# Kernel optimization log

Hardware: AMD Instinct MI355X
Metric: run time of the kernel (lower is better)

Reference implementation:

```python
import jax, jax.numpy as jnp
import numpy as np

NF = 64        # num_feat
B = 4
H = 128
W = 128
KH = KW = 3
K = KH * KW    # 9 kernel taps
DG = 1         # deformable_groups


def conv3x3(x, w, b):
    y = jax.lax.conv_general_dilated(
        x, w, window_strides=(1, 1), padding=((1, 1), (1, 1)),
        dimension_numbers=('NCHW', 'OIHW', 'NCHW'))
    return y + b[None, :, None, None]


def lrelu(x):
    return jnp.where(x >= 0, x, 0.1 * x)


def modulated_deform_conv(x, offset, mask, w, b):
    """DCNv2: bilinear gather at learned offsets, modulated by sigmoid mask.
    x: [B,C,H,W], offset: [B,2K,H,W] (y,x interleaved per tap), mask: [B,K,H,W].
    stride=1, padding=1, dilation=1, zero outside boundaries (mmcv semantics).
    """
    Bb, C, Hh, Ww = x.shape
    off = offset.reshape(Bb, K, 2, Hh, Ww)
    oy, ox = off[:, :, 0], off[:, :, 1]
    ki = (jnp.arange(K) // KW - 1).astype(x.dtype)  # dilation*i - pad
    kj = (jnp.arange(K) % KW - 1).astype(x.dtype)
    py = jnp.arange(Hh, dtype=x.dtype)[None, None, :, None] + ki[None, :, None, None] + oy  # [B,K,H,W]
    px = jnp.arange(Ww, dtype=x.dtype)[None, None, None, :] + kj[None, :, None, None] + ox
    y0 = jnp.floor(py)
    x0 = jnp.floor(px)
    wy1 = py - y0
    wx1 = px - x0
    x_flat = x.reshape(Bb, C, Hh * Ww)

    def gather(yi, xi):
        valid = (yi >= 0) & (yi < Hh) & (xi >= 0) & (xi < Ww)
        yc = jnp.clip(yi, 0, Hh - 1).astype(jnp.int32)
        xc = jnp.clip(xi, 0, Ww - 1).astype(jnp.int32)
        idx = (yc * Ww + xc).reshape(Bb, -1)                      # [B, K*H*W]
        g = jax.vmap(lambda xf, i: jnp.take(xf, i, axis=1))(x_flat, idx)  # [B,C,K*H*W]
        g = g.reshape(Bb, C, K, Hh, Ww)
        return g * valid[:, None].astype(x.dtype)

    v00 = gather(y0, x0)
    v01 = gather(y0, x0 + 1)
    v10 = gather(y0 + 1, x0)
    v11 = gather(y0 + 1, x0 + 1)
    wy = wy1[:, None]
    wx = wx1[:, None]
    samp = (v00 * (1 - wy) * (1 - wx) + v01 * (1 - wy) * wx
            + v10 * wy * (1 - wx) + v11 * wy * wx)                # [B,C,K,H,W]
    samp = samp * mask[:, None]
    out = jnp.einsum('bckhw,ock->bohw', samp, w.reshape(w.shape[0], C, K))
    return out + b[None, :, None, None]


def setup_inputs() -> dict:
    key = jax.random.key(0)
    ks = jax.random.split(key, 12)
    s = 0.05
    return {
        'nbr_feat_l': jax.random.normal(ks[0], (B, NF, H, W), jnp.float32),
        'ref_feat_l': jax.random.normal(ks[1], (B, NF, H, W), jnp.float32),
        'w1': jax.random.normal(ks[2], (NF, 2 * NF, 3, 3), jnp.float32) * s,
        'b1': jnp.zeros((NF,), jnp.float32),
        'w2': jax.random.normal(ks[3], (NF, NF, 3, 3), jnp.float32) * s,
        'b2': jnp.zeros((NF,), jnp.float32),
        'w3': jax.random.normal(ks[4], (NF, NF, 3, 3), jnp.float32) * s,
        'b3': jnp.zeros((NF,), jnp.float32),
        'w_off': jax.random.normal(ks[5], (DG * 3 * K, NF, 3, 3), jnp.float32) * s,
        'b_off': jnp.zeros((DG * 3 * K,), jnp.float32),
        'w_dcn': jax.random.normal(ks[6], (NF, NF, 3, 3), jnp.float32) * s,
        'b_dcn': jnp.zeros((NF,), jnp.float32),
    }


def reference(nbr_feat_l, ref_feat_l, w1, b1, w2, b2, w3, b3, w_off, b_off, w_dcn, b_dcn):
    o = jnp.concatenate([nbr_feat_l, ref_feat_l], axis=1)
    o = lrelu(conv3x3(o, w1, b1))
    o = lrelu(conv3x3(o, w2, b2))
    o = lrelu(conv3x3(o, w3, b3))
    out = conv3x3(o, w_off, b_off)                      # [B, 27, H, W]
    o1, o2, m = jnp.split(out, 3, axis=1)
    offset = 15 * jnp.tanh(jnp.concatenate([o1, o2], axis=1))  # [B, 18, H, W]
    mask = jax.nn.sigmoid(m)                                   # [B, 9, H, W]
    feat = lrelu(modulated_deform_conv(nbr_feat_l, offset, mask, w_dcn, b_dcn))
    return feat, offset, mask
```

## Files before the change

kernel.cpp:

```cpp
#include <hip/hip_runtime.h>
#include <math.h>


typedef _Float16 h8 __attribute__((ext_vector_type(8)));
typedef _Float16 h4 __attribute__((ext_vector_type(4)));
typedef _Float16 h2 __attribute__((ext_vector_type(2)));
typedef float f4 __attribute__((ext_vector_type(4)));

__global__ __launch_bounds__(256) void setup_kernel(
    const float* __restrict__ nbr, const float* __restrict__ refp,
    const float* __restrict__ w1, const float* __restrict__ w2,
    const float* __restrict__ w3, const float* __restrict__ w_off,
    const float* __restrict__ w_dcn,
    _Float16* __restrict__ X1, _Float16* __restrict__ X2,
    _Float16* __restrict__ B64, _Float16* __restrict__ C64,
    _Float16* __restrict__ wF1, _Float16* __restrict__ wF2,
    _Float16* __restrict__ wF3, _Float16* __restrict__ wFo,
    _Float16* __restrict__ wFd) {
  __shared__ float t[64 * 65];
  int bid = blockIdx.x;
  int tid = threadIdx.x;
  if (bid < 792) {
    int i = bid * 256 + tid;
    if (i < 73728) {
      int j = i;
      int icw = j & 31; int t1 = j >> 5; int oc = t1 & 63; int t2 = t1 >> 6;
      int ch = t2 & 3; int tap = t2 >> 2; int ic = ch * 32 + icw;
      wF1[j] = (_Float16)w1[(oc * 128 + ic) * 9 + tap];
    } else if (i < 110592) {
      int j = i - 73728;
      int icw = j & 31; int t1 = j >> 5; int oc = t1 & 63; int t2 = t1 >> 6;
      int ch = t2 & 1; int tap = t2 >> 1; int ic = ch * 32 + icw;
      wF2[j] = (_Float16)w2[(oc * 64 + ic) * 9 + tap];
    } else if (i < 147456) {
      int j = i - 110592;
      int icw = j & 31; int t1 = j >> 5; int oc = t1 & 63; int t2 = t1 >> 6;
      int ch = t2 & 1; int tap = t2 >> 1; int ic = ch * 32 + icw;
      wF3[j] = (_Float16)w3[(oc * 64 + ic) * 9 + tap];
    } else if (i < 165888) {
      int jj = i - 147456;
      int pc = jj >> 10;
      int mt = (jj >> 9) & 1;
      int Lx = (jj >> 3) & 63;
      int e  = jj & 7;
      int tap = pc >> 1, c = pc & 1;
      int oc = mt * 16 + (Lx & 15);
      int ic = c * 32 + (Lx >> 4) * 8 + e;
      float v = (oc < 27) ? w_off[(oc * 64 + ic) * 9 + tap] : 0.f;
      wFo[jj] = (_Float16)v;
    } else if (i < 202752) {
      int jj = i - 165888;
      int ks = jj >> 11;
      int mt = (jj >> 9) & 3;
      int Lx = (jj >> 3) & 63;
      int e  = jj & 7;
      int k = ks >> 1, s = ks & 1;
      int oc = mt * 16 + (Lx & 15);
      int ch = s * 32 + (Lx >> 4) * 8 + e;
      wFd[jj] = (_Float16)w_dcn[(oc * 64 + ch) * 9 + k];
    }
    return;
  }
  if (bid < 1050) {
    int i = (bid - 792) * 256 + tid;
    int bufi = i / 16512;
    int j = i - bufi * 16512;
    int b = j / 4128;
    int r = j - b * 4128;
    int p = r >> 3; int cg = r & 7;
    int row, col;
    if (p < 130)      { row = 0;   col = p; }
    else if (p < 260) { row = 129; col = p - 130; }
    else if (p < 388) { row = 1 + (p - 260); col = 0; }
    else              { row = 1 + (p - 388); col = 129; }
    _Float16* dst = (bufi == 0) ? X1 : (bufi == 1) ? X2 : (bufi == 2) ? B64 : C64;
    uint4 z; z.x = z.y = z.z = z.w = 0u;
    *(uint4*)(dst + ((size_t)(b * 130 + row) * 130 + col) * 64 + cg * 8) = z;
    return;
  }
  int j = bid - 1050;
  int half = j & 1;
  int y = (j >> 1) & 127;
  int b = (j >> 8) & 3;
  int src = j >> 10;
  const float* sp = src ? refp : nbr;
  _Float16* dst = src ? X2 : X1;
  for (int l = tid; l < 64 * 64; l += 256) {
    int c = l >> 6, gx = l & 63;
    t[c * 65 + gx] = sp[(((size_t)b * 64 + c) << 14) + (y << 7) + half * 64 + gx];
  }
  __syncthreads();
  unsigned* dstU = (unsigned*)dst;
  for (int l = tid; l < 64 * 32; l += 256) {
    int pxl = l >> 5, c2 = l & 31;
    union { _Float16 h[2]; unsigned u; } pk;
    pk.h[0] = (_Float16)t[(2 * c2) * 65 + pxl];
    pk.h[1] = (_Float16)t[(2 * c2 + 1) * 65 + pxl];
    dstU[((size_t)(b * 130 + y + 1) * 130 + 1 + half * 64 + pxl) * 32 + c2] = pk.u;
  }
}

template <int NCH, bool SPLIT>
__global__ __launch_bounds__(128, 4) void conv3x3_lds_kernel(
    const _Float16* __restrict__ X1, const _Float16* __restrict__ X2,
    const _Float16* __restrict__ W, const float* __restrict__ bias,
    _Float16* __restrict__ outP) {
  __shared__ _Float16 Lb[3 * 72 * 64];
  int tid = threadIdx.x;
  int wv = tid >> 6, L = tid & 63;
  int lm = L & 15, lq = L >> 4;
  int bid = blockIdx.x;
  int xcd = bid & 7, j = bid >> 3;
  int half = j & 1;
  int y = (xcd << 4) | ((j >> 1) & 15);
  int b = j >> 5;
  int px0 = half * 64;

  auto stage = [&](const _Float16* Xsrc) {
    const char* Xb = (const char*)Xsrc;
    size_t rb0 = ((size_t)(b * 130 + y) * 130 + px0) * 128;
    for (int i = wv; i < 27; i += 2) {
      int o = i * 1024 + L * 16;
      int row = o / 9216;
      int orow = o - row * 9216;
      int px = orow >> 7;
      int c2 = (orow >> 4) & 7;
      size_t src = rb0 + (size_t)row * 16640 + (size_t)(px << 7) + (((c2 ^ (px & 7))) << 4);
      __builtin_amdgcn_global_load_lds(
          (const __attribute__((address_space(1))) void*)(Xb + src),
          (__attribute__((address_space(3))) void*)((char*)Lb + i * 1024), 16, 0, 0);
    }
  };

  f4 acc[2][4];
#pragma unroll
  for (int m = 0; m < 2; ++m)
#pragma unroll
    for (int n = 0; n < 4; ++n) acc[m][n] = (f4)0.f;

  auto compute = [&](int cbase) {
#pragma unroll
    for (int ci = 0; ci < 2; ++ci) {
      int c = cbase + ci;
#pragma unroll
      for (int tg = 0; tg < 3; ++tg) {
        h8 a[6];
#pragma unroll
        for (int t = 0; t < 3; ++t) {
          int tap = tg * 3 + t;
          const _Float16* wp = W + (size_t)((tap * NCH + c) * 64 + wv * 32 + lm) * 32 + lq * 8;
          a[2 * t]     = *(const h8*)(wp);
          a[2 * t + 1] = *(const h8*)(wp + 512);
        }
#pragma unroll
        for (int t = 0; t < 3; ++t) {
          int tap = tg * 3 + t;
          const int dy = tap / 3, dx = tap % 3;
          h8 bf[4];
#pragma unroll
          for (int g = 0; g < 4; ++g) {
            int pxcol = g * 16 + lm + dx;
            int chunk = (ci * 4 + lq) ^ (pxcol & 7);
            int off = dy * 9216 + (pxcol << 7) + (chunk << 4);
            bf[g] = *(const h8*)((const char*)Lb + off);
          }
#pragma unroll
          for (int g = 0; g < 4; ++g) {
            acc[0][g] = __builtin_amdgcn_mfma_f32_16x16x32_f16(a[2 * t], bf[g], acc[0][g], 0, 0, 0);
            acc[1][g] = __builtin_amdgcn_mfma_f32_16x16x32_f16(a[2 * t + 1], bf[g], acc[1][g], 0, 0, 0);
          }
        }
      }
    }
  };

  stage(X1);
  asm volatile("s_waitcnt vmcnt(0)" ::: "memory");
  __syncthreads();
  compute(0);
  if (SPLIT) {
    __syncthreads();
    stage(X2);
    asm volatile("s_waitcnt vmcnt(0)" ::: "memory");
    __syncthreads();
    compute(2);
  }

  const size_t obase = ((size_t)(b * 130 + (y + 1)) * 130 + 1 + px0) * 64;
#pragma unroll
  for (int mt = 0; mt < 2; ++mt)
#pragma unroll
    for (int nt = 0; nt < 4; ++nt) {
      int px = nt * 16 + lm;
      h4 pk;
#pragma unroll
      for (int r = 0; r < 4; ++r) {
        int oc = wv * 32 + mt * 16 + lq * 4 + r;
        float v = acc[mt][nt][r] + bias[oc];
        v = (v >= 0.f) ? v : 0.1f * v;
        pk[r] = (_Float16)v;
      }
      *(h4*)(outP + obase + (size_t)px * 64 + wv * 32 + mt * 16 + lq * 4) = pk;
    }
}

__global__ __launch_bounds__(256, 4) void off_dcn_kernel(
    const _Float16* __restrict__ Xc, const _Float16* __restrict__ Xs,
    const _Float16* __restrict__ Wo, const float* __restrict__ bo,
    const _Float16* __restrict__ wD, const float* __restrict__ bd,
    float* __restrict__ off_out, float* __restrict__ mask_out,
    float* __restrict__ out) {
  __shared__ float Soff[4][16][28];
  int tid = threadIdx.x;
  int wv = tid >> 6, L = tid & 63;
  int lm = L & 15, lq = L >> 4;
  int lq8 = lq * 8;
  int g = blockIdx.x;
  int xcd = g & 7;
  int r0 = g >> 3;
  int half = r0 & 1;
  int y = (xcd << 4) | ((r0 >> 1) & 15);
  int b = r0 >> 5;
  int px0 = half * 64 + wv * 16;
  int gpx = px0 + lm;
  int hw = (y << 7) + gpx;
  int rb = b * 130;

  {
    f4 oa[2];
    oa[0] = (f4)0.f; oa[1] = (f4)0.f;
#pragma unroll
    for (int c = 0; c < 2; ++c) {
      const void* pB[9];
#pragma unroll
      for (int tap = 0; tap < 9; ++tap) {
        const int dy = tap / 3 - 1, dx = tap % 3 - 1;
        pB[tap] = (const void*)(Xc + ((size_t)((rb + (y + 1 + dy)) * 130) + (1 + dx) + px0 + lm) * 64
                                   + c * 32 + lq8);
      }
      h8 bq[9];
      asm volatile(
          "global_load_dwordx4 %0, %9, off\n\t"
          "global_load_dwordx4 %1, %10, off\n\t"
          "global_load_dwordx4 %2, %11, off\n\t"
          "global_load_dwordx4 %3, %12, off\n\t"
          "global_load_dwordx4 %4, %13, off\n\t"
          "global_load_dwordx4 %5, %14, off\n\t"
          "global_load_dwordx4 %6, %15, off\n\t"
          "global_load_dwordx4 %7, %16, off\n\t"
          "global_load_dwordx4 %8, %17, off\n\t"
          "s_waitcnt vmcnt(0)"
          : "=&v"(bq[0]), "=&v"(bq[1]), "=&v"(bq[2]), "=&v"(bq[3]), "=&v"(bq[4]),
            "=&v"(bq[5]), "=&v"(bq[6]), "=&v"(bq[7]), "=&v"(bq[8])
          : "v"(pB[0]), "v"(pB[1]), "v"(pB[2]), "v"(pB[3]), "v"(pB[4]),
            "v"(pB[5]), "v"(pB[6]), "v"(pB[7]), "v"(pB[8])
          : "memory");
#pragma unroll
      for (int tap = 0; tap < 9; ++tap) {
        const _Float16* wp = Wo + (size_t)(tap * 2 + c) * 1024 + L * 8;
        h8 a0 = *(const h8*)(wp);
        h8 a1 = *(const h8*)(wp + 512);
        oa[0] = __builtin_amdgcn_mfma_f32_16x16x32_f16(a0, bq[tap], oa[0], 0, 0, 0);
        oa[1] = __builtin_amdgcn_mfma_f32_16x16x32_f16(a1, bq[tap], oa[1], 0, 0, 0);
      }
    }
#pragma unroll
    for (int mt = 0; mt < 2; ++mt)
#pragma unroll
      for (int r = 0; r < 4; ++r) {
        int oc = mt * 16 + lq * 4 + r;
        if (oc < 18) {
          float v = 15.f * tanhf(oa[mt][r] + bo[oc]);
          off_out[((b * 18 + oc) << 14) + hw] = v;
          Soff[wv][lm][oc] = v;
        } else if (oc < 27) {
          float v = 1.f / (1.f + expf(-(oa[mt][r] + bo[oc])));
          mask_out[((b * 9 + (oc - 18)) << 14) + hw] = v;
          Soff[wv][lm][oc] = v;
        }
      }
  }

  f4 acc[4];
#pragma unroll
  for (int mm = 0; mm < 4; ++mm) acc[mm] = (f4)0.f;

  const char* Xb = (const char*)Xs;
  const int cbL = lq8 * 2;

#pragma unroll
  for (int gp = 0; gp < 3; ++gp) {
    float soy[3], sox[3], som[3];
#pragma unroll
    for (int t = 0; t < 3; ++t) {
      const int k = gp * 3 + t;
      soy[t] = Soff[wv][lm][2 * k];
      sox[t] = Soff[wv][lm][2 * k + 1];
      som[t] = Soff[wv][lm][18 + k];
    }
    int ro0[3], ro1[3], co0[3], co1[3];
    h2 Wc00[3], Wc01[3], Wc10[3], Wc11[3];
#pragma unroll
    for (int t = 0; t < 3; ++t) {
      const int k = gp * 3 + t;
      const int kr = k / 3, kc = k - kr * 3;
      float py = (float)(y + kr - 1) + soy[t];
      float pxf = (float)(gpx + kc - 1) + sox[t];
      float fy = floorf(py), fx = floorf(pxf);
      float wy = py - fy, wx = pxf - fx;
      int y0 = (int)fy, x0 = (int)fx;
      int y1 = y0 + 1, x1 = x0 + 1;
      float vy0 = ((unsigned)y0 < 128u) ? 1.f : 0.f;
      float vy1 = ((unsigned)y1 < 128u) ? 1.f : 0.f;
      float vx0 = ((unsigned)x0 < 128u) ? 1.f : 0.f;
      float vx1 = ((unsigned)x1 < 128u) ? 1.f : 0.f;
      float ey = 1.f - wy, ex = 1.f - wx;
      float mk = som[t];
      _Float16 w00 = (_Float16)(ey * ex * mk * vy0 * vx0);
      _Float16 w01 = (_Float16)(ey * wx * mk * vy0 * vx1);
      _Float16 w10 = (_Float16)(wy * ex * mk * vy1 * vx0);
      _Float16 w11 = (_Float16)(wy * wx * mk * vy1 * vx1);
      Wc00[t] = (h2){w00, w00}; Wc01[t] = (h2){w01, w01};
      Wc10[t] = (h2){w10, w10}; Wc11[t] = (h2){w11, w11};
      int y0c = min(max(y0, 0), 127) + 1, y1c = min(max(y1, 0), 127) + 1;
      int x0c = min(max(x0, 0), 127) + 1, x1c = min(max(x1, 0), 127) + 1;
      ro0[t] = (rb + y0c) * 16640;
      ro1[t] = (rb + y1c) * 16640;
      co0[t] = x0c * 128;
      co1[t] = x1c * 128;
    }
#pragma unroll
    for (int s = 0; s < 2; ++s) {
      const int cb2 = cbL + s * 64;
      const void* A[12];
#pragma unroll
      for (int t = 0; t < 3; ++t) {
        A[t * 4 + 0] = (const void*)(Xb + (ro0[t] + co0[t] + cb2));
        A[t * 4 + 1] = (const void*)(Xb + (ro0[t] + co1[t] + cb2));
        A[t * 4 + 2] = (const void*)(Xb + (ro1[t] + co0[t] + cb2));
        A[t * 4 + 3] = (const void*)(Xb + (ro1[t] + co1[t] + cb2));
      }
      h8 gv[12];
      asm volatile(
          "global_load_dwordx4 %0, %12, off\n\t"
          "global_load_dwordx4 %1, %13, off\n\t"
          "global_load_dwordx4 %2, %14, off\n\t"
          "global_load_dwordx4 %3, %15, off\n\t"
          "global_load_dwordx4 %4, %16, off\n\t"
          "global_load_dwordx4 %5, %17, off\n\t"
          "global_load_dwordx4 %6, %18, off\n\t"
          "global_load_dwordx4 %7, %19, off\n\t"
          "global_load_dwordx4 %8, %20, off\n\t"
          "global_load_dwordx4 %9, %21, off\n\t"
          "global_load_dwordx4 %10, %22, off\n\t"
          "global_load_dwordx4 %11, %23, off\n\t"
          "s_waitcnt vmcnt(0)"
          : "=&v"(gv[0]), "=&v"(gv[1]), "=&v"(gv[2]), "=&v"(gv[3]),
            "=&v"(gv[4]), "=&v"(gv[5]), "=&v"(gv[6]), "=&v"(gv[7]),
            "=&v"(gv[8]), "=&v"(gv[9]), "=&v"(gv[10]), "=&v"(gv[11])
          : "v"(A[0]), "v"(A[1]), "v"(A[2]), "v"(A[3]),
            "v"(A[4]), "v"(A[5]), "v"(A[6]), "v"(A[7]),
            "v"(A[8]), "v"(A[9]), "v"(A[10]), "v"(A[11])
          : "memory");
#pragma unroll
      for (int t = 0; t < 3; ++t) {
        const int k = gp * 3 + t;
        h8 bv;
#pragma unroll
        for (int j2 = 0; j2 < 4; ++j2) {
          h2 a  = {gv[t * 4 + 0][2 * j2], gv[t * 4 + 0][2 * j2 + 1]};
          h2 bb = {gv[t * 4 + 1][2 * j2], gv[t * 4 + 1][2 * j2 + 1]};
          h2 cc = {gv[t * 4 + 2][2 * j2], gv[t * 4 + 2][2 * j2 + 1]};
          h2 dd = {gv[t * 4 + 3][2 * j2], gv[t * 4 + 3][2 * j2 + 1]};
          h2 r = a * Wc00[t];
          r += bb * Wc01[t];
          r += cc * Wc10[t];
          r += dd * Wc11[t];
          bv[2 * j2] = r[0];
          bv[2 * j2 + 1] = r[1];
        }
        const _Float16* wp = wD + (size_t)(k * 2 + s) * 2048 + L * 8;
        acc[0] = __builtin_amdgcn_mfma_f32_16x16x32_f16(*(const h8*)(wp), bv, acc[0], 0, 0, 0);
        acc[1] = __builtin_amdgcn_mfma_f32_16x16x32_f16(*(const h8*)(wp + 512), bv, acc[1], 0, 0, 0);
        acc[2] = __builtin_amdgcn_mfma_f32_16x16x32_f16(*(const h8*)(wp + 1024), bv, acc[2], 0, 0, 0);
        acc[3] = __builtin_amdgcn_mfma_f32_16x16x32_f16(*(const h8*)(wp + 1536), bv, acc[3], 0, 0, 0);
      }
    }
  }

#pragma unroll
  for (int mt = 0; mt < 4; ++mt)
#pragma unroll
    for (int r = 0; r < 4; ++r) {
      int oc = mt * 16 + lq * 4 + r;
      float v = acc[mt][r] + bd[oc];
      v = (v >= 0.f) ? v : 0.1f * v;
      out[(((b << 6) + oc) << 14) + (y << 7) + gpx] = v;
    }
}

extern "C" void kernel_launch(void* const* d_in, const int* in_sizes, int n_in,
                              void* d_out, int out_size, void* d_ws, size_t ws_size,
                              hipStream_t stream) {
  const float* nbr   = (const float*)d_in[0];
  const float* refp  = (const float*)d_in[1];
  const float* w1    = (const float*)d_in[2];
  const float* b1    = (const float*)d_in[3];
  const float* w2    = (const float*)d_in[4];
  const float* b2    = (const float*)d_in[5];
  const float* w3    = (const float*)d_in[6];
  const float* b3    = (const float*)d_in[7];
  const float* w_off = (const float*)d_in[8];
  const float* b_off = (const float*)d_in[9];
  const float* w_dcn = (const float*)d_in[10];
  const float* b_dcn = (const float*)d_in[11];

  float* outp = (float*)d_out;
  float* feat = outp;
  float* offp = outp + 4194304;
  float* mskp = outp + 4194304 + 1179648;

  char* ws = (char*)d_ws;
  const size_t PB = 8652800;
  _Float16* X1  = (_Float16*)ws;
  _Float16* X2  = (_Float16*)(ws + PB);
  _Float16* B64 = (_Float16*)(ws + 2 * PB);
  _Float16* C64 = (_Float16*)(ws + 3 * PB);
  char* p = ws + 4 * PB;
  _Float16* wF1 = (_Float16*)p;  p += (size_t)73728 * 2;
  _Float16* wF2 = (_Float16*)p;  p += (size_t)36864 * 2;
  _Float16* wF3 = (_Float16*)p;  p += (size_t)36864 * 2;
  _Float16* wFo = (_Float16*)p;  p += (size_t)18432 * 2;
  _Float16* wFd = (_Float16*)p;

  setup_kernel<<<dim3(3098), 256, 0, stream>>>(nbr, refp, w1, w2, w3, w_off, w_dcn,
                                               X1, X2, B64, C64, wF1, wF2, wF3, wFo, wFd);
  conv3x3_lds_kernel<4, true><<<dim3(1024), 128, 0, stream>>>(X1, X2, wF1, b1, B64);
  conv3x3_lds_kernel<2, false><<<dim3(1024), 128, 0, stream>>>(B64, nullptr, wF2, b2, C64);
  conv3x3_lds_kernel<2, false><<<dim3(1024), 128, 0, stream>>>(C64, nullptr, wF3, b3, B64);
  off_dcn_kernel<<<dim3(1024), 256, 0, stream>>>(B64, X1, wFo, b_off, wFd, b_dcn,
                                                 offp, mskp, feat);
}
```

Measured before the change: 202.5 us.

## Pre-swizzle conv weights into MFMA fragment order and restructure DCN gather per tap

Changes the fp16 weight layout for the three 3x3 convs so each lane's A-fragment is contiguous per wave (coalesced 16-byte loads indexed by lane). Also restructures the deformable gather loop to process one tap at a time, issuing both channel halves of each corner as paired loads using an immediate offset instead of batching three taps per load group. This trades memory-level parallelism (8 outstanding loads instead of 12) for lower register pressure and simpler addressing.

```diff
diff --git a/kernel.cpp b/kernel.cpp
--- a/kernel.cpp
+++ b/kernel.cpp
@@ -24,18 +24,27 @@
     int i = bid * 256 + tid;
     if (i < 73728) {
       int j = i;
-      int icw = j & 31; int t1 = j >> 5; int oc = t1 & 63; int t2 = t1 >> 6;
-      int ch = t2 & 3; int tap = t2 >> 2; int ic = ch * 32 + icw;
+      int e = j & 7; int Lx = (j >> 3) & 63; int mt = (j >> 9) & 1; int wvx = (j >> 10) & 1;
+      int pc = j >> 11;
+      int tap = pc >> 2, c = pc & 3;
+      int oc = wvx * 32 + mt * 16 + (Lx & 15);
+      int ic = c * 32 + ((Lx >> 4) << 3) + e;
       wF1[j] = (_Float16)w1[(oc * 128 + ic) * 9 + tap];
     } else if (i < 110592) {
       int j = i - 73728;
-      int icw = j & 31; int t1 = j >> 5; int oc = t1 & 63; int t2 = t1 >> 6;
-      int ch = t2 & 1; int tap = t2 >> 1; int ic = ch * 32 + icw;
+      int e = j & 7; int Lx = (j >> 3) & 63; int mt = (j >> 9) & 1; int wvx = (j >> 10) & 1;
+      int pc = j >> 11;
+      int tap = pc >> 1, c = pc & 1;
+      int oc = wvx * 32 + mt * 16 + (Lx & 15);
+      int ic = c * 32 + ((Lx >> 4) << 3) + e;
       wF2[j] = (_Float16)w2[(oc * 64 + ic) * 9 + tap];
     } else if (i < 147456) {
       int j = i - 110592;
-      int icw = j & 31; int t1 = j >> 5; int oc = t1 & 63; int t2 = t1 >> 6;
-      int ch = t2 & 1; int tap = t2 >> 1; int ic = ch * 32 + icw;
+      int e = j & 7; int Lx = (j >> 3) & 63; int mt = (j >> 9) & 1; int wvx = (j >> 10) & 1;
+      int pc = j >> 11;
+      int tap = pc >> 1, c = pc & 1;
+      int oc = wvx * 32 + mt * 16 + (Lx & 15);
+      int ic = c * 32 + ((Lx >> 4) << 3) + e;
       wF3[j] = (_Float16)w3[(oc * 64 + ic) * 9 + tap];
     } else if (i < 165888) {
       int jj = i - 147456;
@@ -148,7 +157,7 @@
 #pragma unroll
         for (int t = 0; t < 3; ++t) {
           int tap = tg * 3 + t;
-          const _Float16* wp = W + (size_t)((tap * NCH + c) * 64 + wv * 32 + lm) * 32 + lq * 8;
+          const _Float16* wp = W + (size_t)((tap * NCH + c) * 2 + wv) * 1024 + L * 8;
           a[2 * t]     = *(const h8*)(wp);
           a[2 * t + 1] = *(const h8*)(wp + 512);
         }
@@ -289,102 +298,69 @@
   const int cbL = lq8 * 2;
 
 #pragma unroll
-  for (int gp = 0; gp < 3; ++gp) {
-    float soy[3], sox[3], som[3];
-#pragma unroll
-    for (int t = 0; t < 3; ++t) {
-      const int k = gp * 3 + t;
-      soy[t] = Soff[wv][lm][2 * k];
-      sox[t] = Soff[wv][lm][2 * k + 1];
-      som[t] = Soff[wv][lm][18 + k];
-    }
-    int ro0[3], ro1[3], co0[3], co1[3];
-    h2 Wc00[3], Wc01[3], Wc10[3], Wc11[3];
-#pragma unroll
-    for (int t = 0; t < 3; ++t) {
-      const int k = gp * 3 + t;
-      const int kr = k / 3, kc = k - kr * 3;
-      float py = (float)(y + kr - 1) + soy[t];
-      float pxf = (float)(gpx + kc - 1) + sox[t];
-      float fy = floorf(py), fx = floorf(pxf);
-      float wy = py - fy, wx = pxf - fx;
-      int y0 = (int)fy, x0 = (int)fx;
-      int y1 = y0 + 1, x1 = x0 + 1;
-      float vy0 = ((unsigned)y0 < 128u) ? 1.f : 0.f;
-      float vy1 = ((unsigned)y1 < 128u) ? 1.f : 0.f;
-      float vx0 = ((unsigned)x0 < 128u) ? 1.f : 0.f;
-      float vx1 = ((unsigned)x1 < 128u) ? 1.f : 0.f;
-      float ey = 1.f - wy, ex = 1.f - wx;
-      float mk = som[t];
-      _Float16 w00 = (_Float16)(ey * ex * mk * vy0 * vx0);
-      _Float16 w01 = (_Float16)(ey * wx * mk * vy0 * vx1);
-      _Float16 w10 = (_Float16)(wy * ex * mk * vy1 * vx0);
-      _Float16 w11 = (_Float16)(wy * wx * mk * vy1 * vx1);
-      Wc00[t] = (h2){w00, w00}; Wc01[t] = (h2){w01, w01};
-      Wc10[t] = (h2){w10, w10}; Wc11[t] = (h2){w11, w11};
-      int y0c = min(max(y0, 0), 127) + 1, y1c = min(max(y1, 0), 127) + 1;
-      int x0c = min(max(x0, 0), 127) + 1, x1c = min(max(x1, 0), 127) + 1;
-      ro0[t] = (rb + y0c) * 16640;
-      ro1[t] = (rb + y1c) * 16640;
-      co0[t] = x0c * 128;
-      co1[t] = x1c * 128;
-    }
+  for (int k = 0; k < 9; ++k) {
+    const int kr = k / 3, kc = k - kr * 3;
+    float oy = Soff[wv][lm][2 * k];
+    float ox = Soff[wv][lm][2 * k + 1];
+    float mk = Soff[wv][lm][18 + k];
+    float py = (float)(y + kr - 1) + oy;
+    float pxf = (float)(gpx + kc - 1) + ox;
+    float fy = floorf(py), fx = floorf(pxf);
+    float wy = py - fy, wx = pxf - fx;
+    int y0 = (int)fy, x0 = (int)fx;
+    int y1 = y0 + 1, x1 = x0 + 1;
+    float vy0 = ((unsigned)y0 < 128u) ? 1.f : 0.f;
+    float vy1 = ((unsigned)y1 < 128u) ? 1.f : 0.f;
+    float vx0 = ((unsigned)x0 < 128u) ? 1.f : 0.f;
+    float vx1 = ((unsigned)x1 < 128u) ? 1.f : 0.f;
+    float ey = 1.f - wy, ex = 1.f - wx;
+    _Float16 w00 = (_Float16)(ey * ex * mk * vy0 * vx0);
+    _Float16 w01 = (_Float16)(ey * wx * mk * vy0 * vx1);
+    _Float16 w10 = (_Float16)(wy * ex * mk * vy1 * vx0);
+    _Float16 w11 = (_Float16)(wy * wx * mk * vy1 * vx1);
+    h2 W00 = {w00, w00}, W01 = {w01, w01}, W10 = {w10, w10}, W11 = {w11, w11};
+    int y0c = min(max(y0, 0), 127) + 1, y1c = min(max(y1, 0), 127) + 1;
+    int x0c = min(max(x0, 0), 127) + 1, x1c = min(max(x1, 0), 127) + 1;
+    const void* a00 = (const void*)(Xb + (rb + y0c) * 16640 + x0c * 128 + cbL);
+    const void* a01 = (const void*)(Xb + (rb + y0c) * 16640 + x1c * 128 + cbL);
+    const void* a10 = (const void*)(Xb + (rb + y1c) * 16640 + x0c * 128 + cbL);
+    const void* a11 = (const void*)(Xb + (rb + y1c) * 16640 + x1c * 128 + cbL);
+    h8 gv[8];
+    asm volatile(
+        "global_load_dwordx4 %0, %8, off\n\t"
+        "global_load_dwordx4 %1, %8, off offset:64\n\t"
+        "global_load_dwordx4 %2, %9, off\n\t"
+        "global_load_dwordx4 %3, %9, off offset:64\n\t"
+        "global_load_dwordx4 %4, %10, off\n\t"
+        "global_load_dwordx4 %5, %10, off offset:64\n\t"
+        "global_load_dwordx4 %6, %11, off\n\t"
+        "global_load_dwordx4 %7, %11, off offset:64\n\t"
+        "s_waitcnt vmcnt(0)"
+        : "=&v"(gv[0]), "=&v"(gv[1]), "=&v"(gv[2]), "=&v"(gv[3]),
+          "=&v"(gv[4]), "=&v"(gv[5]), "=&v"(gv[6]), "=&v"(gv[7])
+        : "v"(a00), "v"(a01), "v"(a10), "v"(a11)
+        : "memory");
 #pragma unroll
     for (int s = 0; s < 2; ++s) {
-      const int cb2 = cbL + s * 64;
-      const void* A[12];
-#pragma unroll
-      for (int t = 0; t < 3; ++t) {
-        A[t * 4 + 0] = (const void*)(Xb + (ro0[t] + co0[t] + cb2));
-        A[t * 4 + 1] = (const void*)(Xb + (ro0[t] + co1[t] + cb2));
-        A[t * 4 + 2] = (const void*)(Xb + (ro1[t] + co0[t] + cb2));
-        A[t * 4 + 3] = (const void*)(Xb + (ro1[t] + co1[t] + cb2));
-      }
-      h8 gv[12];
-      asm volatile(
-          "global_load_dwordx4 %0, %12, off\n\t"
-          "global_load_dwordx4 %1, %13, off\n\t"
-          "global_load_dwordx4 %2, %14, off\n\t"
-          "global_load_dwordx4 %3, %15, off\n\t"
-          "global_load_dwordx4 %4, %16, off\n\t"
-          "global_load_dwordx4 %5, %17, off\n\t"
-          "global_load_dwordx4 %6, %18, off\n\t"
-          "global_load_dwordx4 %7, %19, off\n\t"
-          "global_load_dwordx4 %8, %20, off\n\t"
-          "global_load_dwordx4 %9, %21, off\n\t"
-          "global_load_dwordx4 %10, %22, off\n\t"
-          "global_load_dwordx4 %11, %23, off\n\t"
-          "s_waitcnt vmcnt(0)"
-          : "=&v"(gv[0]), "=&v"(gv[1]), "=&v"(gv[2]), "=&v"(gv[3]),
-            "=&v"(gv[4]), "=&v"(gv[5]), "=&v"(gv[6]), "=&v"(gv[7]),
-            "=&v"(gv[8]), "=&v"(gv[9]), "=&v"(gv[10]), "=&v"(gv[11])
-          : "v"(A[0]), "v"(A[1]), "v"(A[2]), "v"(A[3]),
-            "v"(A[4]), "v"(A[5]), "v"(A[6]), "v"(A[7]),
-            "v"(A[8]), "v"(A[9]), "v"(A[10]), "v"(A[11])
-          : "memory");
-#pragma unroll
-      for (int t = 0; t < 3; ++t) {
-        const int k = gp * 3 + t;
-        h8 bv;
-#pragma unroll
-        for (int j2 = 0; j2 < 4; ++j2) {
-          h2 a  = {gv[t * 4 + 0][2 * j2], gv[t * 4 + 0][2 * j2 + 1]};
-          h2 bb = {gv[t * 4 + 1][2 * j2], gv[t * 4 + 1][2 * j2 + 1]};
-          h2 cc = {gv[t * 4 + 2][2 * j2], gv[t * 4 + 2][2 * j2 + 1]};
-          h2 dd = {gv[t * 4 + 3][2 * j2], gv[t * 4 + 3][2 * j2 + 1]};
-          h2 r = a * Wc00[t];
-          r += bb * Wc01[t];
-          r += cc * Wc10[t];
-          r += dd * Wc11[t];
-          bv[2 * j2] = r[0];
-          bv[2 * j2 + 1] = r[1];
-        }
-        const _Float16* wp = wD + (size_t)(k * 2 + s) * 2048 + L * 8;
-        acc[0] = __builtin_amdgcn_mfma_f32_16x16x32_f16(*(const h8*)(wp), bv, acc[0], 0, 0, 0);
-        acc[1] = __builtin_amdgcn_mfma_f32_16x16x32_f16(*(const h8*)(wp + 512), bv, acc[1], 0, 0, 0);
-        acc[2] = __builtin_amdgcn_mfma_f32_16x16x32_f16(*(const h8*)(wp + 1024), bv, acc[2], 0, 0, 0);
-        acc[3] = __builtin_amdgcn_mfma_f32_16x16x32_f16(*(const h8*)(wp + 1536), bv, acc[3], 0, 0, 0);
-      }
+      h8 bv;
+#pragma unroll
+      for (int j2 = 0; j2 < 4; ++j2) {
+        h2 a  = {gv[0 + s][2 * j2], gv[0 + s][2 * j2 + 1]};
+        h2 bb = {gv[2 + s][2 * j2], gv[2 + s][2 * j2 + 1]};
+        h2 cc = {gv[4 + s][2 * j2], gv[4 + s][2 * j2 + 1]};
+        h2 dd = {gv[6 + s][2 * j2], gv[6 + s][2 * j2 + 1]};
+        h2 r = a * W00;
+        r += bb * W01;
+        r += cc * W10;
+        r += dd * W11;
+        bv[2 * j2] = r[0];
+        bv[2 * j2 + 1] = r[1];
+      }
+      const _Float16* wp = wD + (size_t)(k * 2 + s) * 2048 + L * 8;
+      acc[0] = __builtin_amdgcn_mfma_f32_16x16x32_f16(*(const h8*)(wp), bv, acc[0], 0, 0, 0);
+      acc[1] = __builtin_amdgcn_mfma_f32_16x16x32_f16(*(const h8*)(wp + 512), bv, acc[1], 0, 0, 0);
+      acc[2] = __builtin_amdgcn_mfma_f32_16x16x32_f16(*(const h8*)(wp + 1024), bv, acc[2], 0, 0, 0);
+      acc[3] = __builtin_amdgcn_mfma_f32_16x16x32_f16(*(const h8*)(wp + 1536), bv, acc[3], 0, 0, 0);
     }
   }
 
```

New measurement: 197.2 us. 1.03x faster.
